# Kernel tuning notes

Hardware: AMD Instinct MI355X
Metric: run time of the kernel (lower is better)

Reference implementation:

```python
import jax, jax.numpy as jnp
import numpy as np

EPS = 1e-6
H = 16  # num_heads


def _layernorm(x):
    m = jnp.mean(x, axis=-1, keepdims=True)
    v = jnp.mean((x - m) ** 2, axis=-1, keepdims=True)
    return (x - m) * jax.lax.rsqrt(v + EPS)


def _rmsnorm(x, scale):
    return x * jax.lax.rsqrt(jnp.mean(x * x, axis=-1, keepdims=True) + EPS) * scale


def _modulation(vec, w, b):
    # vec: [B, D] -> 6 tensors of [B, 1, D]
    out = jax.nn.silu(vec) @ w + b
    return jnp.split(out[:, None, :], 6, axis=-1)


def _qkv_heads(x, w):
    # x: [B, L, D] -> q,k,v each [B, H, L, Dh]  (rearrange 'B L (K H D) -> K B H L D')
    B, L, _ = x.shape
    qkv = (x @ w).reshape(B, L, 3, H, -1)
    qkv = jnp.transpose(qkv, (2, 0, 3, 1, 4))
    return qkv[0], qkv[1], qkv[2]


def _apply_rope(xq, xk, pe):
    # pe: [B, 1, L, Dh//2, 2, 2]
    shp = xq.shape
    xq_ = xq.reshape(*shp[:-1], -1, 1, 2)
    xk_ = xk.reshape(*shp[:-1], -1, 1, 2)
    xq_out = pe[..., 0] * xq_[..., 0] + pe[..., 1] * xq_[..., 1]
    xk_out = pe[..., 0] * xk_[..., 0] + pe[..., 1] * xk_[..., 1]
    return xq_out.reshape(shp), xk_out.reshape(shp)


def _attention(q, k, v, pe):
    q, k = _apply_rope(q, k, pe)
    scale = q.shape[-1] ** -0.5
    logits = jnp.einsum('bhqd,bhkd->bhqk', q, k) * scale
    probs = jax.nn.softmax(logits, axis=-1)
    x = jnp.einsum('bhqk,bhkd->bhqd', probs, v)
    B, h, L, Dh = x.shape
    return jnp.transpose(x, (0, 2, 1, 3)).reshape(B, L, h * Dh)


def reference(obs, cond, vec, pe,
              obs_mod_w, obs_mod_b, obs_qkv_w, obs_q_scale, obs_k_scale,
              obs_proj_w, obs_proj_b, obs_mlp_w1, obs_mlp_b1, obs_mlp_w2, obs_mlp_b2,
              cond_mod_w, cond_mod_b, cond_qkv_w, cond_q_scale, cond_k_scale,
              cond_proj_w, cond_proj_b, cond_mlp_w1, cond_mlp_b1, cond_mlp_w2, cond_mlp_b2):
    o_shift1, o_scale1, o_gate1, o_shift2, o_scale2, o_gate2 = _modulation(vec, obs_mod_w, obs_mod_b)
    c_shift1, c_scale1, c_gate1, c_shift2, c_scale2, c_gate2 = _modulation(vec, cond_mod_w, cond_mod_b)

    obs_m = (1 + o_scale1) * _layernorm(obs) + o_shift1
    oq, ok, ov = _qkv_heads(obs_m, obs_qkv_w)
    oq = _rmsnorm(oq, obs_q_scale)
    ok = _rmsnorm(ok, obs_k_scale)

    cond_m = (1 + c_scale1) * _layernorm(cond) + c_shift1
    cq, ck, cv = _qkv_heads(cond_m, cond_qkv_w)
    cq = _rmsnorm(cq, cond_q_scale)
    ck = _rmsnorm(ck, cond_k_scale)

    q = jnp.concatenate((cq, oq), axis=2)
    k = jnp.concatenate((ck, ok), axis=2)
    v = jnp.concatenate((cv, ov), axis=2)
    attn = _attention(q, k, v, pe)
    Lc = cond.shape[1]
    cond_attn, obs_attn = attn[:, :Lc], attn[:, Lc:]

    obs = obs + o_gate1 * (obs_attn @ obs_proj_w + obs_proj_b)
    h_obs = (1 + o_scale2) * _layernorm(obs) + o_shift2
    obs = obs + o_gate2 * (jax.nn.gelu(h_obs @ obs_mlp_w1 + obs_mlp_b1, approximate=True) @ obs_mlp_w2 + obs_mlp_b2)

    cond = cond + c_gate1 * (cond_attn @ cond_proj_w + cond_proj_b)
    h_cond = (1 + c_scale2) * _layernorm(cond) + c_shift2
    cond = cond + c_gate2 * (jax.nn.gelu(h_cond @ cond_mlp_w1 + cond_mlp_b1, approximate=True) @ cond_mlp_w2 + cond_mlp_b2)
    return obs, cond


def setup_inputs() -> dict:
    key = jax.random.key(0)
    ks = jax.random.split(key, 24)
    D, Dh, Mh = 1024, 64, 4096
    Lo, Lc = 3072, 1024
    B = 1
    s = 0.02
    inp = {
        'obs': jax.random.normal(ks[0], (B, Lo, D), jnp.float32),
        'cond': jax.random.normal(ks[1], (B, Lc, D), jnp.float32),
        'vec': jax.random.normal(ks[2], (B, D), jnp.float32),
        'pe': jax.random.normal(ks[3], (B, 1, Lo + Lc, Dh // 2, 2, 2), jnp.float32),
        'obs_mod_w': jax.random.normal(ks[4], (D, 6 * D), jnp.float32) * s,
        'obs_mod_b': jax.random.normal(ks[5], (6 * D,), jnp.float32) * s,
        'obs_qkv_w': jax.random.normal(ks[6], (D, 3 * D), jnp.float32) * s,
        'obs_q_scale': jnp.ones((Dh,), jnp.float32),
        'obs_k_scale': jnp.ones((Dh,), jnp.float32),
        'obs_proj_w': jax.random.normal(ks[7], (D, D), jnp.float32) * s,
        'obs_proj_b': jax.random.normal(ks[8], (D,), jnp.float32) * s,
        'obs_mlp_w1': jax.random.normal(ks[9], (D, Mh), jnp.float32) * s,
        'obs_mlp_b1': jax.random.normal(ks[10], (Mh,), jnp.float32) * s,
        'obs_mlp_w2': jax.random.normal(ks[11], (Mh, D), jnp.float32) * s,
        'obs_mlp_b2': jax.random.normal(ks[12], (D,), jnp.float32) * s,
        'cond_mod_w': jax.random.normal(ks[13], (D, 6 * D), jnp.float32) * s,
        'cond_mod_b': jax.random.normal(ks[14], (6 * D,), jnp.float32) * s,
        'cond_qkv_w': jax.random.normal(ks[15], (D, 3 * D), jnp.float32) * s,
        'cond_q_scale': jnp.ones((Dh,), jnp.float32),
        'cond_k_scale': jnp.ones((Dh,), jnp.float32),
        'cond_proj_w': jax.random.normal(ks[16], (D, D), jnp.float32) * s,
        'cond_proj_b': jax.random.normal(ks[17], (D,), jnp.float32) * s,
        'cond_mlp_w1': jax.random.normal(ks[18], (D, Mh), jnp.float32) * s,
        'cond_mlp_b1': jax.random.normal(ks[19], (Mh,), jnp.float32) * s,
        'cond_mlp_w2': jax.random.normal(ks[20], (Mh, D), jnp.float32) * s,
        'cond_mlp_b2': jax.random.normal(ks[21], (D,), jnp.float32) * s,
    }
    return inp
```

## Files before the change

### kernel.cpp

```cpp
#include <hip/hip_runtime.h>

typedef unsigned short u16;
typedef __bf16 bf16x8 __attribute__((ext_vector_type(8)));
typedef __bf16 bf16x4 __attribute__((ext_vector_type(4)));
typedef float f32x4 __attribute__((ext_vector_type(4)));
typedef unsigned int u32x4 __attribute__((ext_vector_type(4)));

#define GLOAD_LDS16(g, l)                                                    \
  __builtin_amdgcn_global_load_lds(                                          \
      (const __attribute__((address_space(1))) void*)(g),                    \
      (__attribute__((address_space(3))) void*)(l), 16, 0, 0)

__device__ __forceinline__ u16 f2bf(float f) {
  unsigned int u = __float_as_uint(f);
  u += 0x7fffu + ((u >> 16) & 1u);
  return (u16)(u >> 16);
}
__device__ __forceinline__ float bf2f(u16 h) {
  return __uint_as_float(((unsigned int)h) << 16);
}
__device__ __forceinline__ unsigned int pack_bf2(float a, float b) {
  return (__float_as_uint(b) & 0xffff0000u) | (__float_as_uint(a) >> 16);
}
__device__ __forceinline__ float fexp2(float x) {
#if __has_builtin(__builtin_amdgcn_exp2f)
  return __builtin_amdgcn_exp2f(x);
#else
  return exp2f(x);
#endif
}
__device__ __forceinline__ float gelu_tanh(float x) {
  float u = 0.7978845608028654f * (x + 0.044715f * x * x * x);
  float e = fexp2(-2.8853900817779268f * fabsf(u));
  float t = (1.0f - e) / (1.0f + e);
  t = (u >= 0.0f) ? t : -t;
  return 0.5f * x * (1.0f + t);
}
__device__ __forceinline__ float silu_f(float v) {
  return v / (1.0f + fexp2(-1.4426950408889634f * v));
}
__device__ __forceinline__ f32x4 mfma16(bf16x8 a, bf16x8 b, f32x4 c) {
  return __builtin_amdgcn_mfma_f32_16x16x32_bf16(a, b, c, 0, 0, 0);
}

__global__ __launch_bounds__(256) void modulation_kernel(
    const float* __restrict__ vec,
    const float* __restrict__ w_o, const float* __restrict__ b_o,
    const float* __restrict__ w_c, const float* __restrict__ b_c,
    float* __restrict__ o_mod, float* __restrict__ c_mod) {
  __shared__ float sv[1024];
  __shared__ float red[256];
  const int tid = threadIdx.x;
  const bool isobs = blockIdx.x < 96;
  const float* w = isobs ? w_o : w_c;
  const float* b = isobs ? b_o : b_c;
  float* out = isobs ? o_mod : c_mod;
  const int jb = (isobs ? blockIdx.x : blockIdx.x - 96) * 64;
  const int col = tid & 63, sl = tid >> 6;
  for (int i = tid; i < 1024; i += 256) {
    sv[i] = silu_f(vec[i]);
  }
  __syncthreads();
  float acc = 0.0f;
  const int kb = sl * 256;
  for (int k = 0; k < 256; ++k)
    acc += sv[kb + k] * w[(size_t)(kb + k) * 6144 + jb + col];
  red[tid] = acc;
  __syncthreads();
  if (sl == 0)
    out[jb + col] = red[col] + red[col + 64] + red[col + 128] + red[col + 192] + b[jb + col];
}

__global__ __launch_bounds__(256) void ln_mod_kernel(
    const float* __restrict__ xc, const float* __restrict__ xo,
    const float* __restrict__ modc, const float* __restrict__ modo,
    int mod_off, u16* __restrict__ out) {
  const int row = blockIdx.x, tid = threadIdx.x;
  const bool is_c = row < 1024;
  const float* x = is_c ? (xc + (size_t)row * 1024) : (xo + (size_t)(row - 1024) * 1024);
  const float* mod = (is_c ? modc : modo) + mod_off;
  float4 v = *(const float4*)(x + tid * 4);
  float s1 = v.x + v.y + v.z + v.w;
  float s2 = v.x * v.x + v.y * v.y + v.z * v.z + v.w * v.w;
#pragma unroll
  for (int m = 1; m < 64; m <<= 1) {
    s1 += __shfl_xor(s1, m);
    s2 += __shfl_xor(s2, m);
  }
  __shared__ float red[8];
  const int w = tid >> 6;
  if ((tid & 63) == 0) { red[w] = s1; red[4 + w] = s2; }
  __syncthreads();
  s1 = red[0] + red[1] + red[2] + red[3];
  s2 = red[4] + red[5] + red[6] + red[7];
  const float mean = s1 * (1.0f / 1024.0f);
  const float var = s2 * (1.0f / 1024.0f) - mean * mean;
  const float rstd = rsqrtf(var + 1e-6f);
  const int d = tid * 4;
  float vv[4] = {v.x, v.y, v.z, v.w};
  ushort4 ov;
  u16* po = (u16*)&ov;
#pragma unroll
  for (int i = 0; i < 4; ++i) {
    float y = (vv[i] - mean) * rstd;
    po[i] = f2bf((1.0f + mod[1024 + d + i]) * y + mod[d + i]);
  }
  *(ushort4*)(out + (size_t)row * 1024 + d) = ov;
}

__global__ __launch_bounds__(256) void ln_mod_b_kernel(
    const u16* __restrict__ x,
    const float* __restrict__ modc, const float* __restrict__ modo,
    int mod_off, u16* __restrict__ out) {
  const int row = blockIdx.x, tid = threadIdx.x;
  const bool is_c = row < 1024;
  const float* mod = (is_c ? modc : modo) + mod_off;
  ushort4 rv = *(const ushort4*)(x + (size_t)row * 1024 + tid * 4);
  float vv[4] = {bf2f(rv.x), bf2f(rv.y), bf2f(rv.z), bf2f(rv.w)};
  float s1 = vv[0] + vv[1] + vv[2] + vv[3];
  float s2 = vv[0] * vv[0] + vv[1] * vv[1] + vv[2] * vv[2] + vv[3] * vv[3];
#pragma unroll
  for (int m = 1; m < 64; m <<= 1) {
    s1 += __shfl_xor(s1, m);
    s2 += __shfl_xor(s2, m);
  }
  __shared__ float red[8];
  const int w = tid >> 6;
  if ((tid & 63) == 0) { red[w] = s1; red[4 + w] = s2; }
  __syncthreads();
  s1 = red[0] + red[1] + red[2] + red[3];
  s2 = red[4] + red[5] + red[6] + red[7];
  const float mean = s1 * (1.0f / 1024.0f);
  const float var = s2 * (1.0f / 1024.0f) - mean * mean;
  const float rstd = rsqrtf(var + 1e-6f);
  const int d = tid * 4;
  ushort4 ov;
  u16* po = (u16*)&ov;
#pragma unroll
  for (int i = 0; i < 4; ++i) {
    float y = (vv[i] - mean) * rstd;
    po[i] = f2bf((1.0f + mod[1024 + d + i]) * y + mod[d + i]);
  }
  *(ushort4*)(out + (size_t)row * 1024 + d) = ov;
}

__global__ __launch_bounds__(256) void transcast_kernel(
    const float* __restrict__ src_c, const float* __restrict__ src_o,
    u16* __restrict__ dst_c, u16* __restrict__ dst_o, int K, int N) {
  const float* src = blockIdx.z ? src_o : src_c;
  u16* dst = blockIdx.z ? dst_o : dst_c;
  const int n0 = blockIdx.x * 64, k0 = blockIdx.y * 64;
  __shared__ float s[64][65];
  const int tid = threadIdx.x;
  const int r = tid >> 4, c4 = (tid & 15) << 2;
#pragma unroll
  for (int p = 0; p < 4; ++p) {
    int kk = r + p * 16;
    float4 v = *(const float4*)(src + (size_t)(k0 + kk) * N + n0 + c4);
    s[kk][c4] = v.x; s[kk][c4 + 1] = v.y; s[kk][c4 + 2] = v.z; s[kk][c4 + 3] = v.w;
  }
  __syncthreads();
#pragma unroll
  for (int p = 0; p < 4; ++p) {
    int nr = r + p * 16;
    ushort4 ov;
    ov.x = f2bf(s[c4 + 0][nr]); ov.y = f2bf(s[c4 + 1][nr]);
    ov.z = f2bf(s[c4 + 2][nr]); ov.w = f2bf(s[c4 + 3][nr]);
    *(ushort4*)(dst + (size_t)(n0 + nr) * K + k0 + c4) = ov;
  }
}

template <int BN>
__global__ __launch_bounds__(256) void gemm_bf16(
    const u16* __restrict__ A, const u16* __restrict__ BTc, const u16* __restrict__ BTo,
    int N, int K, int mode,
    const float* __restrict__ bias_c, const float* __restrict__ bias_o,
    const float* __restrict__ gate_c, const float* __restrict__ gate_o,
    const float* __restrict__ x0_c, const float* __restrict__ x0_o,
    const u16* __restrict__ x1, void* __restrict__ outp,
    u16* __restrict__ oq, u16* __restrict__ ok, u16* __restrict__ ov) {
  constexpr int MI = (BN == 128) ? 4 : 2;
  __shared__ u16 As[128 * 32];
  __shared__ u16 Bs[BN * 32];
  const int tid = threadIdx.x;
  const int m0 = blockIdx.y * 128, n0 = blockIdx.x * BN;
  const bool is_c = (m0 < 1024);
  const u16* __restrict__ BT = is_c ? BTc : BTo;
  const int w = tid >> 6, lane = tid & 63, quad = lane >> 4, ln = lane & 15;
  const int wm = (BN == 128) ? (w >> 1) * 64 : w * 32;
  const int wn = (BN == 128) ? (w & 1) * 64 : 0;
  f32x4 acc[MI][4] = {};
  const int nkt = K >> 5;
  for (int kt = 0; kt < nkt; ++kt) {
    __syncthreads();
    {
      int c = tid;
      GLOAD_LDS16(A + (size_t)(m0 + (c >> 2)) * K + kt * 32 + (c & 3) * 8, As + c * 8);
      c = tid + 256;
      GLOAD_LDS16(A + (size_t)(m0 + (c >> 2)) * K + kt * 32 + (c & 3) * 8, As + c * 8);
      c = tid;
      GLOAD_LDS16(BT + (size_t)(n0 + (c >> 2)) * K + kt * 32 + (c & 3) * 8, Bs + c * 8);
      if (BN == 128) {
        c = tid + 256;
        GLOAD_LDS16(BT + (size_t)(n0 + (c >> 2)) * K + kt * 32 + (c & 3) * 8, Bs + c * 8);
      }
    }
    __syncthreads();
    bf16x8 a[MI], b[4];
#pragma unroll
    for (int i = 0; i < MI; ++i)
      a[i] = *(const bf16x8*)(As + (wm + i * 16 + ln) * 32 + quad * 8);
#pragma unroll
    for (int j = 0; j < 4; ++j)
      b[j] = *(const bf16x8*)(Bs + (wn + j * 16 + ln) * 32 + quad * 8);
#pragma unroll
    for (int i = 0; i < MI; ++i)
#pragma unroll
      for (int j = 0; j < 4; ++j) acc[i][j] = mfma16(a[i], b[j], acc[i][j]);
  }
  const float* bias = is_c ? bias_c : bias_o;
  const float* gate = is_c ? gate_c : gate_o;
  const float* x0 = is_c ? x0_c : x0_o;
#pragma unroll
  for (int i = 0; i < MI; ++i) {
#pragma unroll
    for (int j = 0; j < 4; ++j) {
#pragma unroll
      for (int r = 0; r < 4; ++r) {
        const int row = m0 + wm + i * 16 + quad * 4 + r;
        const int col = n0 + wn + j * 16 + ln;
        const float v = acc[i][j][r];
        if (mode == 0) {
          const int which = col >> 10, hh = (col & 1023) >> 6, dd = col & 63;
          u16* dst = (which == 0) ? oq : (which == 1) ? ok : ov;
          dst[((size_t)hh * 4096 + row) * 64 + dd] = f2bf(v);
        } else if (mode == 1) {
          const float xv = is_c ? x0[(size_t)row * 1024 + col]
                                : x0[(size_t)(row - 1024) * 1024 + col];
          ((u16*)outp)[(size_t)row * 1024 + col] = f2bf(xv + gate[col] * (v + bias[col]));
        } else if (mode == 2) {
          ((u16*)outp)[(size_t)row * N + col] = f2bf(gelu_tanh(v + bias[col]));
        } else {
          const float res = bf2f(x1[(size_t)row * 1024 + col]);
          const float val = res + gate[col] * (v + bias[col]);
          const size_t oidx = (row < 1024)
              ? (size_t)3145728 + (size_t)row * 1024 + col
              : (size_t)(row - 1024) * 1024 + col;
          ((float*)outp)[oidx] = val;
        }
      }
    }
  }
}

__global__ __launch_bounds__(256) void qkprep_kernel(
    const float* __restrict__ pe,
    const float* __restrict__ qs_c, const float* __restrict__ ks_c,
    const float* __restrict__ qs_o, const float* __restrict__ ks_o,
    u16* __restrict__ qraw, u16* __restrict__ kraw) {
  const int l = blockIdx.x, tid = threadIdx.x;
  const bool is_c = l < 1024;
  const float* qs = is_c ? qs_c : qs_o;
  const float* ks = is_c ? ks_c : ks_o;
  const int head = tid >> 4, dd = (tid * 4) & 63;
  const size_t off = ((size_t)head * 4096 + l) * 64 + dd;
  const float* peb = pe + (size_t)l * 128 + (size_t)dd * 2;
  float4 pe0 = *(const float4*)(peb);
  float4 pe1 = *(const float4*)(peb + 4);
  {
    ushort4 raw = *(const ushort4*)(qraw + off);
    float x0 = bf2f(raw.x), x1v = bf2f(raw.y), x2 = bf2f(raw.z), x3 = bf2f(raw.w);
    float ssq = x0 * x0 + x1v * x1v + x2 * x2 + x3 * x3;
#pragma unroll
    for (int m = 1; m < 16; m <<= 1) ssq += __shfl_xor(ssq, m);
    float rms = rsqrtf(ssq * (1.0f / 64.0f) + 1e-6f) * 0.18033688011112042f;
    float n0 = x0 * rms * qs[dd + 0], n1 = x1v * rms * qs[dd + 1];
    float n2 = x2 * rms * qs[dd + 2], n3 = x3 * rms * qs[dd + 3];
    ushort4 o;
    o.x = f2bf(pe0.x * n0 + pe0.y * n1);
    o.y = f2bf(pe0.z * n0 + pe0.w * n1);
    o.z = f2bf(pe1.x * n2 + pe1.y * n3);
    o.w = f2bf(pe1.z * n2 + pe1.w * n3);
    *(ushort4*)(qraw + off) = o;
  }
  {
    ushort4 raw = *(const ushort4*)(kraw + off);
    float x0 = bf2f(raw.x), x1v = bf2f(raw.y), x2 = bf2f(raw.z), x3 = bf2f(raw.w);
    float ssq = x0 * x0 + x1v * x1v + x2 * x2 + x3 * x3;
#pragma unroll
    for (int m = 1; m < 16; m <<= 1) ssq += __shfl_xor(ssq, m);
    float rms = rsqrtf(ssq * (1.0f / 64.0f) + 1e-6f);
    float n0 = x0 * rms * ks[dd + 0], n1 = x1v * rms * ks[dd + 1];
    float n2 = x2 * rms * ks[dd + 2], n3 = x3 * rms * ks[dd + 3];
    ushort4 o;
    o.x = f2bf(pe0.x * n0 + pe0.y * n1);
    o.y = f2bf(pe0.z * n0 + pe0.w * n1);
    o.z = f2bf(pe1.x * n2 + pe1.y * n3);
    o.w = f2bf(pe1.z * n2 + pe1.w * n3);
    *(ushort4*)(kraw + off) = o;
  }
}

__global__ __launch_bounds__(256) void vtrans_kernel(
    const u16* __restrict__ vh, u16* __restrict__ vt) {
  const int h = blockIdx.y, k0 = blockIdx.x * 64;
  __shared__ u16 s[64 * 66];
  const int tid = threadIdx.x;
#pragma unroll
  for (int st = 0; st < 2; ++st) {
    int c = tid + st * 256;
    int row = c >> 3, off = (c & 7) << 3;
    ushort4 v0 = *(const ushort4*)(vh + ((size_t)h * 4096 + k0 + row) * 64 + off);
    ushort4 v1 = *(const ushort4*)(vh + ((size_t)h * 4096 + k0 + row) * 64 + off + 4);
    u16* p = s + row * 66 + off;
    p[0] = v0.x; p[1] = v0.y; p[2] = v0.z; p[3] = v0.w;
    p[4] = v1.x; p[5] = v1.y; p[6] = v1.z; p[7] = v1.w;
  }
  __syncthreads();
#pragma unroll
  for (int st = 0; st < 2; ++st) {
    int c = tid + st * 256;
    int dd = c >> 3, kk = (c & 7) << 3;
    ushort4 a, b;
    a.x = s[(kk + 0) * 66 + dd]; a.y = s[(kk + 1) * 66 + dd];
    a.z = s[(kk + 2) * 66 + dd]; a.w = s[(kk + 3) * 66 + dd];
    b.x = s[(kk + 4) * 66 + dd]; b.y = s[(kk + 5) * 66 + dd];
    b.z = s[(kk + 6) * 66 + dd]; b.w = s[(kk + 7) * 66 + dd];
    u16* o = vt + ((size_t)h * 64 + dd) * 4096 + k0 + kk;
    *(ushort4*)(o) = a;
    *(ushort4*)(o + 4) = b;
  }
}

__device__ __forceinline__ void attn_chunk(
    int cn, const u16* kbase, const u16* vbase,
    int w, int ln, int quad, int kperm,
    const bf16x8 (&bq)[4][2],
    bf16x8 (&akc)[2][2], bf16x8 (&bvc)[4],
    bf16x8 (&akn)[2][2], bf16x8 (&bvn)[4],
    f32x4 (&o)[4][4], float (&rs)[4]) {
  constexpr int L = 4096;
  if (cn < 32) {
    const int kbn = cn * 128 + w * 32;
#pragma unroll
    for (int kk = 0; kk < 2; ++kk)
#pragma unroll
      for (int hf = 0; hf < 2; ++hf)
        akn[kk][hf] = *(const bf16x8*)(kbase + (size_t)(kbn + kperm + kk * 4) * 64 + hf * 32 + quad * 8);
#pragma unroll
    for (int jd = 0; jd < 4; ++jd)
      bvn[jd] = *(const bf16x8*)(vbase + (size_t)(jd * 16 + ln) * L + kbn + quad * 8);
  }
  f32x4 sT[2][4] = {};
#pragma unroll
  for (int kk = 0; kk < 2; ++kk)
#pragma unroll
    for (int nq = 0; nq < 4; ++nq) {
      sT[kk][nq] = mfma16(akc[kk][0], bq[nq][0], sT[kk][nq]);
      sT[kk][nq] = mfma16(akc[kk][1], bq[nq][1], sT[kk][nq]);
    }
#pragma unroll
  for (int nq = 0; nq < 4; ++nq) {
    u32x4 pw;
#pragma unroll
    for (int kk = 0; kk < 2; ++kk) {
      float p0 = fexp2(sT[kk][nq][0]);
      float p1 = fexp2(sT[kk][nq][1]);
      float p2 = fexp2(sT[kk][nq][2]);
      float p3 = fexp2(sT[kk][nq][3]);
      rs[nq] += (p0 + p1) + (p2 + p3);
      pw[kk * 2 + 0] = pack_bf2(p0, p1);
      pw[kk * 2 + 1] = pack_bf2(p2, p3);
    }
    const bf16x8 ap = __builtin_bit_cast(bf16x8, pw);
#pragma unroll
    for (int jd = 0; jd < 4; ++jd)
      o[nq][jd] = mfma16(ap, bvc[jd], o[nq][jd]);
  }
}

__global__ __launch_bounds__(256) void attn_kernel(
    const u16* __restrict__ qh, const u16* __restrict__ kh,
    const u16* __restrict__ vt, u16* __restrict__ attn) {
  constexpr int L = 4096;
  const int h = blockIdx.y;
  const int q0 = blockIdx.x * 64;
  const int tid = threadIdx.x, w = tid >> 6, lane = tid & 63;
  const int quad = lane >> 4, ln = lane & 15;
  __shared__ __align__(16) char smem[35840];
  float* bufA = (float*)smem;
  float* bufB = bufA + 4352;
  float* rs4 = bufB + 4352;

  bf16x8 bq[4][2];
  const u16* qbase = qh + ((size_t)h * L + q0) * 64;
#pragma unroll
  for (int nq = 0; nq < 4; ++nq)
#pragma unroll
    for (int hf = 0; hf < 2; ++hf)
      bq[nq][hf] = *(const bf16x8*)(qbase + (nq * 16 + ln) * 64 + hf * 32 + quad * 8);

  f32x4 o[4][4] = {};
  float rs[4] = {0.f, 0.f, 0.f, 0.f};
  const u16* kbase = kh + (size_t)h * L * 64;
  const u16* vbase = vt + (size_t)h * 64 * L;
  const int kperm = ((ln >> 2) << 3) + (ln & 3);

  bf16x8 akA[2][2], akB[2][2], bvA[4], bvB[4];
  {
    const int kb0 = w * 32;
#pragma unroll
    for (int kk = 0; kk < 2; ++kk)
#pragma unroll
      for (int hf = 0; hf < 2; ++hf)
        akA[kk][hf] = *(const bf16x8*)(kbase + (size_t)(kb0 + kperm + kk * 4) * 64 + hf * 32 + quad * 8);
#pragma unroll
    for (int jd = 0; jd < 4; ++jd)
      bvA[jd] = *(const bf16x8*)(vbase + (size_t)(jd * 16 + ln) * L + kb0 + quad * 8);
  }
  for (int c = 0; c < 32; c += 2) {
    attn_chunk(c + 1, kbase, vbase, w, ln, quad, kperm, bq, akA, bvA, akB, bvB, o, rs);
    attn_chunk(c + 2, kbase, vbase, w, ln, quad, kperm, bq, akB, bvB, akA, bvA, o, rs);
  }

  __syncthreads();
#pragma unroll
  for (int nq = 0; nq < 4; ++nq) {
    rs[nq] += __shfl_xor(rs[nq], 16);
    rs[nq] += __shfl_xor(rs[nq], 32);
  }
  if (quad == 0) {
#pragma unroll
    for (int nq = 0; nq < 4; ++nq) rs4[w * 64 + nq * 16 + ln] = rs[nq];
  }
  if (w == 1) {
#pragma unroll
    for (int nq = 0; nq < 4; ++nq)
#pragma unroll
      for (int jd = 0; jd < 4; ++jd)
        *(f32x4*)(bufA + (jd * 16 + ln) * 68 + nq * 16 + quad * 4) = o[nq][jd];
  }
  if (w == 3) {
#pragma unroll
    for (int nq = 0; nq < 4; ++nq)
#pragma unroll
      for (int jd = 0; jd < 4; ++jd)
        *(f32x4*)(bufB + (jd * 16 + ln) * 68 + nq * 16 + quad * 4) = o[nq][jd];
  }
  __syncthreads();
  if (w == 0) {
#pragma unroll
    for (int nq = 0; nq < 4; ++nq)
#pragma unroll
      for (int jd = 0; jd < 4; ++jd)
        o[nq][jd] += *(const f32x4*)(bufA + (jd * 16 + ln) * 68 + nq * 16 + quad * 4);
  }
  if (w == 2) {
#pragma unroll
    for (int nq = 0; nq < 4; ++nq)
#pragma unroll
      for (int jd = 0; jd < 4; ++jd)
        o[nq][jd] += *(const f32x4*)(bufB + (jd * 16 + ln) * 68 + nq * 16 + quad * 4);
  }
  __syncthreads();
  if (w == 2) {
#pragma unroll
    for (int nq = 0; nq < 4; ++nq)
#pragma unroll
      for (int jd = 0; jd < 4; ++jd)
        *(f32x4*)(bufA + (jd * 16 + ln) * 68 + nq * 16 + quad * 4) = o[nq][jd];
  }
  __syncthreads();
  if (w == 0) {
    float linv[4][4];
#pragma unroll
    for (int nq = 0; nq < 4; ++nq)
#pragma unroll
      for (int r = 0; r < 4; ++r) {
        const int qr = nq * 16 + quad * 4 + r;
        linv[nq][r] = 1.0f / (rs4[qr] + rs4[64 + qr] + rs4[128 + qr] + rs4[192 + qr]);
      }
#pragma unroll
    for (int nq = 0; nq < 4; ++nq)
#pragma unroll
      for (int jd = 0; jd < 4; ++jd) {
        f32x4 of = o[nq][jd];
        of += *(const f32x4*)(bufA + (jd * 16 + ln) * 68 + nq * 16 + quad * 4);
#pragma unroll
        for (int r = 0; r < 4; ++r) {
          const int row = q0 + nq * 16 + quad * 4 + r;
          attn[(size_t)row * 1024 + h * 64 + jd * 16 + ln] = f2bf(of[r] * linv[nq][r]);
        }
      }
  }
}

extern "C" void kernel_launch(void* const* d_in, const int* in_sizes, int n_in,
                              void* d_out, int out_size, void* d_ws, size_t ws_size,
                              hipStream_t stream) {
  (void)in_sizes; (void)n_in; (void)out_size; (void)ws_size;
  const float* obs         = (const float*)d_in[0];
  const float* cond        = (const float*)d_in[1];
  const float* vec         = (const float*)d_in[2];
  const float* pe          = (const float*)d_in[3];
  const float* obs_mod_w   = (const float*)d_in[4];
  const float* obs_mod_b   = (const float*)d_in[5];
  const float* obs_qkv_w   = (const float*)d_in[6];
  const float* obs_q_scale = (const float*)d_in[7];
  const float* obs_k_scale = (const float*)d_in[8];
  const float* obs_proj_w  = (const float*)d_in[9];
  const float* obs_proj_b  = (const float*)d_in[10];
  const float* obs_mlp_w1  = (const float*)d_in[11];
  const float* obs_mlp_b1  = (const float*)d_in[12];
  const float* obs_mlp_w2  = (const float*)d_in[13];
  const float* obs_mlp_b2  = (const float*)d_in[14];
  const float* cond_mod_w  = (const float*)d_in[15];
  const float* cond_mod_b  = (const float*)d_in[16];
  const float* cond_qkv_w  = (const float*)d_in[17];
  const float* cond_q_scale= (const float*)d_in[18];
  const float* cond_k_scale= (const float*)d_in[19];
  const float* cond_proj_w = (const float*)d_in[20];
  const float* cond_proj_b = (const float*)d_in[21];
  const float* cond_mlp_w1 = (const float*)d_in[22];
  const float* cond_mlp_b1 = (const float*)d_in[23];
  const float* cond_mlp_w2 = (const float*)d_in[24];
  const float* cond_mlp_b2 = (const float*)d_in[25];

  char* ws = (char*)d_ws;
  float* o_mod = (float*)ws;
  float* c_mod = o_mod + 6144;
  char* base = ws + 65536;
  u16* qkvT_c  = (u16*)base;
  u16* qkvT_o  = (u16*)(base + 6291456);
  u16* projT_c = (u16*)base;
  u16* projT_o = (u16*)(base + 2097152);
  u16* mlp1T_c = (u16*)base;
  u16* mlp1T_o = (u16*)(base + 8388608);
  u16* mlp2T_c = (u16*)base;
  u16* mlp2T_o = (u16*)(base + 8388608);
  u16* xm   = (u16*)(base + 16777216);
  u16* x1   = (u16*)(base + 16777216);
  u16* qraw = (u16*)(base + 25165824);
  u16* hm   = (u16*)(base + 25165824);
  u16* kraw = (u16*)(base + 33554432);
  u16* vraw = (u16*)(base + 41943040);
  u16* vt   = (u16*)(base + 50331648);
  u16* attn = (u16*)(base + 58720256);
  u16* g    = (u16*)(base + 33554432);

  modulation_kernel<<<192, 256, 0, stream>>>(vec, obs_mod_w, obs_mod_b,
                                             cond_mod_w, cond_mod_b, o_mod, c_mod);
  ln_mod_kernel<<<4096, 256, 0, stream>>>(cond, obs, c_mod, o_mod, 0, xm);
  transcast_kernel<<<dim3(48, 16, 2), 256, 0, stream>>>(cond_qkv_w, obs_qkv_w,
                                                        qkvT_c, qkvT_o, 1024, 3072);
  gemm_bf16<128><<<dim3(24, 32), 256, 0, stream>>>(xm, qkvT_c, qkvT_o, 3072, 1024, 0,
      nullptr, nullptr, nullptr, nullptr, nullptr, nullptr, nullptr, nullptr,
      qraw, kraw, vraw);
  qkprep_kernel<<<4096, 256, 0, stream>>>(pe, cond_q_scale, cond_k_scale,
                                          obs_q_scale, obs_k_scale, qraw, kraw);
  vtrans_kernel<<<dim3(64, 16), 256, 0, stream>>>(vraw, vt);
  attn_kernel<<<dim3(64, 16), 256, 0, stream>>>(qraw, kraw, vt, attn);
  transcast_kernel<<<dim3(16, 16, 2), 256, 0, stream>>>(cond_proj_w, obs_proj_w,
                                                        projT_c, projT_o, 1024, 1024);
  gemm_bf16<64><<<dim3(16, 32), 256, 0, stream>>>(attn, projT_c, projT_o, 1024, 1024, 1,
      cond_proj_b, obs_proj_b, c_mod + 2048, o_mod + 2048, cond, obs,
      nullptr, (void*)x1, nullptr, nullptr, nullptr);
  ln_mod_b_kernel<<<4096, 256, 0, stream>>>(x1, c_mod, o_mod, 3072, hm);
  transcast_kernel<<<dim3(64, 16, 2), 256, 0, stream>>>(cond_mlp_w1, obs_mlp_w1,
                                                        mlp1T_c, mlp1T_o, 1024, 4096);
  gemm_bf16<128><<<dim3(32, 32), 256, 0, stream>>>(hm, mlp1T_c, mlp1T_o, 4096, 1024, 2,
      cond_mlp_b1, obs_mlp_b1, nullptr, nullptr, nullptr, nullptr,
      nullptr, (void*)g, nullptr, nullptr, nullptr);
  transcast_kernel<<<dim3(16, 64, 2), 256, 0, stream>>>(cond_mlp_w2, obs_mlp_w2,
                                                        mlp2T_c, mlp2T_o, 4096, 1024);
  gemm_bf16<64><<<dim3(16, 32), 256, 0, stream>>>(g, mlp2T_c, mlp2T_o, 1024, 4096, 3,
      cond_mlp_b2, obs_mlp_b2, c_mod + 5120, o_mod + 5120, nullptr, nullptr,
      x1, d_out, nullptr, nullptr, nullptr);
}
```

Baseline: 648.4 us.

## Pre-pack K and V into MFMA fragment order for contiguous attention loads

qkprep and vtrans now write K and V into a packed layout that matches the per-lane MFMA fragment order, one 512-element block per chunk, wave and sub-tile. The attention inner loop then loads each fragment as a contiguous lane*8 offset instead of strided row or column gathers, which is meant to cut memory transactions and address arithmetic. vtrans now runs before qkprep, because kpack reuses the vraw buffer region and V has to be consumed first. This adds index math in the prep kernels and depends on that buffer aliasing order.

```diff
diff --git a/kernel.cpp b/kernel.cpp
--- a/kernel.cpp
+++ b/kernel.cpp
@@ -257,7 +257,7 @@
     const float* __restrict__ pe,
     const float* __restrict__ qs_c, const float* __restrict__ ks_c,
     const float* __restrict__ qs_o, const float* __restrict__ ks_o,
-    u16* __restrict__ qraw, u16* __restrict__ kraw) {
+    u16* __restrict__ qraw, u16* __restrict__ kraw, u16* __restrict__ kpack) {
   const int l = blockIdx.x, tid = threadIdx.x;
   const bool is_c = l < 1024;
   const float* qs = is_c ? qs_c : qs_o;
@@ -297,12 +297,17 @@
     o.y = f2bf(pe0.z * n0 + pe0.w * n1);
     o.z = f2bf(pe1.x * n2 + pe1.y * n3);
     o.w = f2bf(pe1.z * n2 + pe1.w * n3);
-    *(ushort4*)(kraw + off) = o;
+    const int cck = l >> 7, wvk = (l >> 5) & 3, rk = l & 31;
+    const int kkk = (rk >> 2) & 1, lnk = ((rk >> 3) << 2) | (rk & 3);
+    const int hfk = dd >> 5, qdk = (dd >> 3) & 3, j0k = dd & 7;
+    u16* kdst = kpack + (size_t)head * 262144
+        + (size_t)((((cck * 4 + wvk) * 4 + kkk * 2 + hfk) * 64 + qdk * 16 + lnk) * 8 + j0k);
+    *(ushort4*)kdst = o;
   }
 }
 
 __global__ __launch_bounds__(256) void vtrans_kernel(
-    const u16* __restrict__ vh, u16* __restrict__ vt) {
+    const u16* __restrict__ vh, u16* __restrict__ vpack) {
   const int h = blockIdx.y, k0 = blockIdx.x * 64;
   __shared__ u16 s[64 * 66];
   const int tid = threadIdx.x;
@@ -326,30 +331,32 @@
     a.z = s[(kk + 2) * 66 + dd]; a.w = s[(kk + 3) * 66 + dd];
     b.x = s[(kk + 4) * 66 + dd]; b.y = s[(kk + 5) * 66 + dd];
     b.z = s[(kk + 6) * 66 + dd]; b.w = s[(kk + 7) * 66 + dd];
-    u16* o = vt + ((size_t)h * 64 + dd) * 4096 + k0 + kk;
+    const int K0 = k0 + kk;
+    const int cc = K0 >> 7, wv = (K0 >> 5) & 3, qd = (K0 >> 3) & 3;
+    const int jd = dd >> 4, lnn = dd & 15;
+    u16* o = vpack + (size_t)h * 262144
+        + (size_t)((((cc * 4 + wv) * 4 + jd) * 64 + qd * 16 + lnn) * 8);
     *(ushort4*)(o) = a;
     *(ushort4*)(o + 4) = b;
   }
 }
 
 __device__ __forceinline__ void attn_chunk(
-    int cn, const u16* kbase, const u16* vbase,
-    int w, int ln, int quad, int kperm,
+    int cn, const u16* kpB, const u16* vpB, int w, int lane,
     const bf16x8 (&bq)[4][2],
     bf16x8 (&akc)[2][2], bf16x8 (&bvc)[4],
     bf16x8 (&akn)[2][2], bf16x8 (&bvn)[4],
     f32x4 (&o)[4][4], float (&rs)[4]) {
-  constexpr int L = 4096;
   if (cn < 32) {
-    const int kbn = cn * 128 + w * 32;
+    const int cb = (cn * 4 + w) * 4;
 #pragma unroll
     for (int kk = 0; kk < 2; ++kk)
 #pragma unroll
       for (int hf = 0; hf < 2; ++hf)
-        akn[kk][hf] = *(const bf16x8*)(kbase + (size_t)(kbn + kperm + kk * 4) * 64 + hf * 32 + quad * 8);
+        akn[kk][hf] = *(const bf16x8*)(kpB + ((cb + kk * 2 + hf) << 9) + lane * 8);
 #pragma unroll
     for (int jd = 0; jd < 4; ++jd)
-      bvn[jd] = *(const bf16x8*)(vbase + (size_t)(jd * 16 + ln) * L + kbn + quad * 8);
+      bvn[jd] = *(const bf16x8*)(vpB + ((cb + jd) << 9) + lane * 8);
   }
   f32x4 sT[2][4] = {};
 #pragma unroll
@@ -380,8 +387,8 @@
 }
 
 __global__ __launch_bounds__(256) void attn_kernel(
-    const u16* __restrict__ qh, const u16* __restrict__ kh,
-    const u16* __restrict__ vt, u16* __restrict__ attn) {
+    const u16* __restrict__ qh, const u16* __restrict__ kp,
+    const u16* __restrict__ vp, u16* __restrict__ attn) {
   constexpr int L = 4096;
   const int h = blockIdx.y;
   const int q0 = blockIdx.x * 64;
@@ -402,25 +409,24 @@
 
   f32x4 o[4][4] = {};
   float rs[4] = {0.f, 0.f, 0.f, 0.f};
-  const u16* kbase = kh + (size_t)h * L * 64;
-  const u16* vbase = vt + (size_t)h * 64 * L;
-  const int kperm = ((ln >> 2) << 3) + (ln & 3);
+  const u16* kpB = kp + (size_t)h * 262144;
+  const u16* vpB = vp + (size_t)h * 262144;
 
   bf16x8 akA[2][2], akB[2][2], bvA[4], bvB[4];
   {
-    const int kb0 = w * 32;
+    const int cb = w * 4;
 #pragma unroll
     for (int kk = 0; kk < 2; ++kk)
 #pragma unroll
       for (int hf = 0; hf < 2; ++hf)
-        akA[kk][hf] = *(const bf16x8*)(kbase + (size_t)(kb0 + kperm + kk * 4) * 64 + hf * 32 + quad * 8);
+        akA[kk][hf] = *(const bf16x8*)(kpB + ((cb + kk * 2 + hf) << 9) + lane * 8);
 #pragma unroll
     for (int jd = 0; jd < 4; ++jd)
-      bvA[jd] = *(const bf16x8*)(vbase + (size_t)(jd * 16 + ln) * L + kb0 + quad * 8);
+      bvA[jd] = *(const bf16x8*)(vpB + ((cb + jd) << 9) + lane * 8);
   }
   for (int c = 0; c < 32; c += 2) {
-    attn_chunk(c + 1, kbase, vbase, w, ln, quad, kperm, bq, akA, bvA, akB, bvB, o, rs);
-    attn_chunk(c + 2, kbase, vbase, w, ln, quad, kperm, bq, akB, bvB, akA, bvA, o, rs);
+    attn_chunk(c + 1, kpB, vpB, w, lane, bq, akA, bvA, akB, bvB, o, rs);
+    attn_chunk(c + 2, kpB, vpB, w, lane, bq, akB, bvB, akA, bvA, o, rs);
   }
 
   __syncthreads();
@@ -544,7 +550,8 @@
   u16* hm   = (u16*)(base + 25165824);
   u16* kraw = (u16*)(base + 33554432);
   u16* vraw = (u16*)(base + 41943040);
-  u16* vt   = (u16*)(base + 50331648);
+  u16* kpack= (u16*)(base + 41943040);
+  u16* vpack= (u16*)(base + 50331648);
   u16* attn = (u16*)(base + 58720256);
   u16* g    = (u16*)(base + 33554432);
 
@@ -556,10 +563,10 @@
   gemm_bf16<128><<<dim3(24, 32), 256, 0, stream>>>(xm, qkvT_c, qkvT_o, 3072, 1024, 0,
       nullptr, nullptr, nullptr, nullptr, nullptr, nullptr, nullptr, nullptr,
       qraw, kraw, vraw);
+  vtrans_kernel<<<dim3(64, 16), 256, 0, stream>>>(vraw, vpack);
   qkprep_kernel<<<4096, 256, 0, stream>>>(pe, cond_q_scale, cond_k_scale,
-                                          obs_q_scale, obs_k_scale, qraw, kraw);
-  vtrans_kernel<<<dim3(64, 16), 256, 0, stream>>>(vraw, vt);
-  attn_kernel<<<dim3(64, 16), 256, 0, stream>>>(qraw, kraw, vt, attn);
+                                          obs_q_scale, obs_k_scale, qraw, kraw, kpack);
+  attn_kernel<<<dim3(64, 16), 256, 0, stream>>>(qraw, kpack, vpack, attn);
   transcast_kernel<<<dim3(16, 16, 2), 256, 0, stream>>>(cond_proj_w, obs_proj_w,
                                                         projT_c, projT_o, 1024, 1024);
   gemm_bf16<64><<<dim3(16, 32), 256, 0, stream>>>(attn, projT_c, projT_o, 1024, 1024, 1,
```

Result: faster. 633.6 us (-2.3%).
